# Kernel optimization log

Measured on AMD Instinct MI355X. Metric: run time of the kernel, lower is better.

The kernel has to match this reference:

```python
import jax, jax.numpy as jnp
import numpy as np

EPS = 1e-5

def _layernorm(x, g, b):
    mu = jnp.mean(x, axis=-1, keepdims=True)
    var = jnp.mean(jnp.square(x - mu), axis=-1, keepdims=True)
    return (x - mu) / jnp.sqrt(var + EPS) * g + b

def setup_inputs() -> dict:
    key = jax.random.key(0)
    ks = jax.random.split(key, 8)
    B, T, E, H, Dh, F = 4, 2048, 1024, 16, 64, 4096
    s = lambda fan: 1.0 / np.sqrt(fan)
    return {
        "x":  jax.random.normal(ks[0], (B, T, E), jnp.float32),
        "Wq": jax.random.normal(ks[1], (H, E, Dh), jnp.float32) * s(E),
        "Wk": jax.random.normal(ks[2], (H, E, Dh), jnp.float32) * s(E),
        "Wv": jax.random.normal(ks[3], (H, E, Dh), jnp.float32) * s(E),
        "Wo": jax.random.normal(ks[4], (E, E), jnp.float32) * s(E),
        "bo": jnp.zeros((E,), jnp.float32),
        "W1": jax.random.normal(ks[5], (E, F), jnp.float32) * s(E),
        "b1": jnp.zeros((F,), jnp.float32),
        "W2": jax.random.normal(ks[6], (F, E), jnp.float32) * s(F),
        "b2": jnp.zeros((E,), jnp.float32),
        "g1": jnp.ones((E,), jnp.float32),
        "bt1": jnp.zeros((E,), jnp.float32),
        "g2": jnp.ones((E,), jnp.float32),
        "bt2": jnp.zeros((E,), jnp.float32),
    }

def reference(x, Wq, Wk, Wv, Wo, bo, W1, b1, W2, b2, g1, bt1, g2, bt2):
    B, T, E = x.shape
    # --- pre-LN multi-head attention (dropout = identity in eval) ---
    h = _layernorm(x, g1, bt1)
    q = jnp.einsum('btc,hcd->bhtd', h, Wq)
    k = jnp.einsum('btc,hcd->bhtd', h, Wk)
    v = jnp.einsum('btc,hcd->bhtd', h, Wv)
    # NOTE: original scales by embed_size**-0.5 (input channel c), not head_size
    scores = jnp.einsum('bhtd,bhsd->bhts', q, k) * (E ** -0.5)
    causal = jnp.tril(jnp.ones((T, T), bool))
    scores = jnp.where(causal, scores, -jnp.inf)
    attn = jax.nn.softmax(scores, axis=-1)
    ctx = jnp.einsum('bhts,bhsd->bhtd', attn, v)
    ctx = ctx.transpose(0, 2, 1, 3).reshape(B, T, E)  # concat heads
    x = x + ctx @ Wo + bo
    # --- pre-LN feed-forward ---
    h2 = _layernorm(x, g2, bt2)
    x = x + jax.nn.relu(h2 @ W1 + b1) @ W2 + b2
    return x
```

## Files before the change

### kernel.cpp

```cpp
#include <hip/hip_runtime.h>

typedef unsigned short u16;
typedef __attribute__((ext_vector_type(8))) short bf16x8;
typedef __attribute__((ext_vector_type(4))) short bf16x4;
typedef __attribute__((ext_vector_type(4))) float f32x4;

#define LOG2E 1.4426950408889634f

__device__ __forceinline__ float b2f(u16 u) {
  union { unsigned int i; float f; } x; x.i = ((unsigned int)u) << 16; return x.f;
}
__device__ __forceinline__ u16 f2b(float f) {
  unsigned int i = __float_as_uint(f);
  unsigned int r = (i + 0x7FFFu + ((i >> 16) & 1u)) >> 16;
  return (u16)r;
}
__device__ __forceinline__ u16 f2bc(float f) {
  return (u16)((__float_as_uint(f) + 0x8000u) >> 16);
}
__device__ __forceinline__ void stc(u16* C, size_t i, float v) { C[i] = f2b(v); }
__device__ __forceinline__ void stc(float* C, size_t i, float v) { C[i] = v; }

__device__ __forceinline__ bool is_f32(const unsigned* probe) {
  return probe[0] == 0x3F800000u;
}
__device__ __forceinline__ float ldin(const void* p, size_t i, bool f32) {
  return f32 ? ((const float*)p)[i] : b2f(((const u16*)p)[i]);
}

__device__ __forceinline__ void gld_lds16(const void* g, void* l) {
  __builtin_amdgcn_global_load_lds(
      (const __attribute__((address_space(1))) unsigned int*)g,
      (__attribute__((address_space(3))) unsigned int*)l, 16, 0, 0);
}

__device__ __forceinline__ void lds_wave_fence() {
  __asm__ volatile("s_waitcnt lgkmcnt(0)" ::: "memory");
}

__device__ __forceinline__ void tr8(unsigned a[4], int lane) {
  unsigned p0, p1, p2, p3;
  p0 = __shfl_xor((int)a[0], 1, 64); p1 = __shfl_xor((int)a[1], 1, 64);
  p2 = __shfl_xor((int)a[2], 1, 64); p3 = __shfl_xor((int)a[3], 1, 64);
  unsigned sel = (lane & 1) ? 0x3276u : 0x5410u;
  a[0] = __byte_perm(a[0], p0, sel); a[1] = __byte_perm(a[1], p1, sel);
  a[2] = __byte_perm(a[2], p2, sel); a[3] = __byte_perm(a[3], p3, sel);
  p0 = __shfl_xor((int)a[0], 2, 64); p1 = __shfl_xor((int)a[1], 2, 64);
  p2 = __shfl_xor((int)a[2], 2, 64); p3 = __shfl_xor((int)a[3], 2, 64);
  if (lane & 2) { a[0] = p1; a[2] = p3; } else { a[1] = p0; a[3] = p2; }
  p0 = __shfl_xor((int)a[0], 4, 64); p1 = __shfl_xor((int)a[1], 4, 64);
  p2 = __shfl_xor((int)a[2], 4, 64); p3 = __shfl_xor((int)a[3], 4, 64);
  if (lane & 4) { a[0] = p2; a[1] = p3; } else { a[2] = p0; a[3] = p1; }
}

struct KV { bf16x8 k0, k1; unsigned va[4], vb[4]; };
__device__ __forceinline__ void load_kv(const u16* __restrict__ qkv, size_t b3072,
                                        int h, int s0, int tid, int w, int lane, KV& t) {
  t.k0 = *(const bf16x8*)(qkv + b3072 + (size_t)(s0 + (tid >> 3)) * 3072 + 1024 + h * 64 + (tid & 7) * 8);
  t.k1 = *(const bf16x8*)(qkv + b3072 + (size_t)(s0 + 32 + (tid >> 3)) * 3072 + 1024 + h * 64 + (tid & 7) * 8);
  const u16* vs = qkv + b3072 + (size_t)(s0 + lane) * 3072 + 2048 + h * 64 + w * 16;
  *(bf16x8*)t.va = *(const bf16x8*)vs;
  *(bf16x8*)t.vb = *(const bf16x8*)(vs + 8);
}

__global__ __launch_bounds__(256) void ln_kernel(
    const void* __restrict__ x, int x_raw,
    const void* __restrict__ g, const void* __restrict__ b,
    u16* __restrict__ y, const unsigned* __restrict__ probe) {
  __shared__ float red[4];
  const bool f32 = is_f32(probe);
  int row = blockIdx.x, tid = threadIdx.x;
  int w = tid >> 6;
  float f0, f1, f2, f3;
  if (x_raw && f32) {
    const float* xr = (const float*)x + (size_t)row * 1024 + tid * 4;
    float4 v = *(const float4*)xr;
    f0 = v.x; f1 = v.y; f2 = v.z; f3 = v.w;
  } else {
    const u16* xr = (const u16*)x + (size_t)row * 1024 + tid * 4;
    bf16x4 v = *(const bf16x4*)xr;
    f0 = b2f((u16)v[0]); f1 = b2f((u16)v[1]); f2 = b2f((u16)v[2]); f3 = b2f((u16)v[3]);
  }
  float s = f0 + f1 + f2 + f3;
  #pragma unroll
  for (int o = 32; o >= 1; o >>= 1) s += __shfl_xor(s, o, 64);
  if ((tid & 63) == 0) red[w] = s;
  __syncthreads();
  float mean = (red[0] + red[1] + red[2] + red[3]) * (1.0f / 1024.0f);
  __syncthreads();
  float d0 = f0 - mean, d1 = f1 - mean, d2 = f2 - mean, d3 = f3 - mean;
  float vs = d0 * d0 + d1 * d1 + d2 * d2 + d3 * d3;
  #pragma unroll
  for (int o = 32; o >= 1; o >>= 1) vs += __shfl_xor(vs, o, 64);
  if ((tid & 63) == 0) red[w] = vs;
  __syncthreads();
  float var = (red[0] + red[1] + red[2] + red[3]) * (1.0f / 1024.0f);
  float rstd = rsqrtf(var + 1e-5f);
  int c = tid * 4;
  float o0 = d0 * rstd * ldin(g, c + 0, f32) + ldin(b, c + 0, f32);
  float o1 = d1 * rstd * ldin(g, c + 1, f32) + ldin(b, c + 1, f32);
  float o2 = d2 * rstd * ldin(g, c + 2, f32) + ldin(b, c + 2, f32);
  float o3 = d3 * rstd * ldin(g, c + 3, f32) + ldin(b, c + 3, f32);
  bf16x4 ov; ov[0] = (short)f2b(o0); ov[1] = (short)f2b(o1);
  ov[2] = (short)f2b(o2); ov[3] = (short)f2b(o3);
  *(bf16x4*)(y + (size_t)row * 1024 + c) = ov;
}

__global__ __launch_bounds__(256) void repack_t(
    const void* __restrict__ src, u16* __restrict__ dst, int N, int K,
    const unsigned* __restrict__ probe) {
  const bool f32 = is_f32(probe);
  int flat = blockIdx.x * 256 + threadIdx.x;
  int n = flat % N;
  int c0 = (flat / N) * 8;
  bf16x8 t;
  #pragma unroll
  for (int j = 0; j < 8; j++) t[j] = (short)f2b(ldin(src, (size_t)(c0 + j) * N + n, f32));
  *(bf16x8*)&dst[(size_t)n * K + c0] = t;
}

__global__ __launch_bounds__(256) void repack_qkv(
    const void* __restrict__ Wq, const void* __restrict__ Wk,
    const void* __restrict__ Wv, u16* __restrict__ dst,
    const unsigned* __restrict__ probe) {
  const bool f32 = is_f32(probe);
  int flat = blockIdx.x * 256 + threadIdx.x;
  int n = flat % 3072;
  int c0 = (flat / 3072) * 8;
  const void* W = (n < 1024) ? Wq : (n < 2048) ? Wk : Wv;
  int nn = n & 1023;
  int hn = nn >> 6, d = nn & 63;
  bf16x8 t;
  #pragma unroll
  for (int j = 0; j < 8; j++)
    t[j] = (short)f2b(ldin(W, (size_t)hn * 65536 + (size_t)(c0 + j) * 64 + d, f32));
  *(bf16x8*)&dst[(size_t)n * 1024 + c0] = t;
}

template <int EPI, typename CT>
__global__ __launch_bounds__(256) void gemm_bt(
    const u16* __restrict__ A, const u16* __restrict__ Bt, CT* __restrict__ C,
    int M, int N, int K, const void* __restrict__ bias,
    const void* __restrict__ res, int res_raw,
    const unsigned* __restrict__ probe) {
  __shared__ __align__(16) u16 sA[128 * 32];
  __shared__ __align__(16) u16 sB[128 * 32];
  const bool f32 = is_f32(probe);
  int tid = threadIdx.x;
  int w = tid >> 6, lane = tid & 63;
  int l15 = lane & 15, q4 = lane >> 4;
  int bm = blockIdx.x * 128, bn = blockIdx.y * 128;
  int wm = (w & 1) * 64, wn = (w >> 1) * 64;
  f32x4 acc[4][4] = {};
  for (int k0 = 0; k0 < K; k0 += 32) {
    #pragma unroll
    for (int j = 0; j < 2; ++j) {
      int c = j * 256 + tid;
      int row = c >> 2, ck = (c & 3) * 8;
      gld_lds16(A + (size_t)(bm + row) * K + k0 + ck, &sA[c * 8]);
    }
    #pragma unroll
    for (int j = 0; j < 2; ++j) {
      int c = j * 256 + tid;
      int row = c >> 2, ck = (c & 3) * 8;
      gld_lds16(Bt + (size_t)(bn + row) * K + k0 + ck, &sB[c * 8]);
    }
    __syncthreads();
    bf16x8 af[4], bf[4];
    #pragma unroll
    for (int i = 0; i < 4; i++) af[i] = *(const bf16x8*)&sA[(wm + i * 16 + l15) * 32 + q4 * 8];
    #pragma unroll
    for (int j = 0; j < 4; j++) bf[j] = *(const bf16x8*)&sB[(wn + j * 16 + l15) * 32 + q4 * 8];
    #pragma unroll
    for (int i = 0; i < 4; i++)
      #pragma unroll
      for (int j = 0; j < 4; j++)
        acc[i][j] = __builtin_amdgcn_mfma_f32_16x16x32_bf16(af[i], bf[j], acc[i][j], 0, 0, 0);
    __syncthreads();
  }
  #pragma unroll
  for (int i = 0; i < 4; i++) {
    int rg = bm + wm + i * 16 + q4 * 4;
    #pragma unroll
    for (int j = 0; j < 4; j++) {
      int cg = bn + wn + j * 16 + l15;
      float bv = (EPI > 0) ? ldin(bias, cg, f32) : 0.0f;
      #pragma unroll
      for (int r = 0; r < 4; r++) {
        float v = acc[i][j][r];
        if (EPI == 1) v += bv + ldin(res, (size_t)(rg + r) * N + cg, res_raw && f32);
        if (EPI == 2) { v += bv; v = fmaxf(v, 0.0f); }
        stc(C, (size_t)(rg + r) * N + cg, v);
      }
    }
  }
}

__global__ __launch_bounds__(256, 4) void attn_kernel(
    const u16* __restrict__ qkv, u16* __restrict__ ctx, int T) {
  __shared__ __align__(16) u16 sK[64 * 68];
  __shared__ __align__(16) u16 sVt[80 * 68];
  __shared__ __align__(16) u16 sP[4 * 16 * 68];
  int tid = threadIdx.x;
  int w = tid >> 6, lane = tid & 63;
  int l15 = lane & 15, q4 = lane >> 4;
  int n = blockIdx.x;
  int qp = n & 15, h = (n >> 4) & 15, b = n >> 8;
  size_t b3072 = (size_t)(b * T) * 3072;
  int pbase = w * 1088;
  const float C = 0.03125f * LOG2E;

  for (int i = tid; i < 16 * 64; i += 256)
    sVt[(64 + (i >> 6)) * 68 + (i & 63)] = 0x3F80;

  KV cur, nxt;
  load_kv(qkv, b3072, h, 0, tid, w, lane, cur);

  for (int half = 0; half < 2; ++half) {
    int qt = half ? (31 - qp) : qp;
    int mb = qt * 64 + w * 16;
    bf16x8 qf0, qf1;
    {
      const u16* qr = qkv + b3072 + (size_t)(mb + l15) * 3072 + h * 64;
      qf0 = *(const bf16x8*)(qr + q4 * 8);
      qf1 = *(const bf16x8*)(qr + 32 + q4 * 8);
    }
    f32x4 o[5] = {};
    int L = qt + 1;
    for (int kt = 0; kt < L; ++kt) {
      int s0 = kt * 64;
      __syncthreads();
      *(bf16x8*)&sK[(tid >> 3) * 68 + (tid & 7) * 8] = cur.k0;
      *(bf16x8*)&sK[(32 + (tid >> 3)) * 68 + (tid & 7) * 8] = cur.k1;
      tr8(cur.va, lane); tr8(cur.vb, lane);
      {
        int dd = w * 16 + (lane & 7), t0 = (lane >> 3) * 8;
        *(bf16x8*)&sVt[dd * 68 + t0] = *(bf16x8*)cur.va;
        *(bf16x8*)&sVt[(dd + 8) * 68 + t0] = *(bf16x8*)cur.vb;
      }
      __syncthreads();
      int ns0 = (kt + 1 < L) ? s0 + 64 : 0;
      load_kv(qkv, b3072, h, ns0, tid, w, lane, nxt);

      bool diag = (kt == qt);
      #pragma unroll
      for (int j = 0; j < 4; ++j) {
        bf16x8 k0 = *(const bf16x8*)&sK[(j * 16 + l15) * 68 + q4 * 8];
        bf16x8 k1 = *(const bf16x8*)&sK[(j * 16 + l15) * 68 + 32 + q4 * 8];
        f32x4 z = {0.f, 0.f, 0.f, 0.f};
        z = __builtin_amdgcn_mfma_f32_16x16x32_bf16(qf0, k0, z, 0, 0, 0);
        z = __builtin_amdgcn_mfma_f32_16x16x32_bf16(qf1, k1, z, 0, 0, 0);
        #pragma unroll
        for (int r = 0; r < 4; ++r) {
          float p = __builtin_amdgcn_exp2f(z[r] * C);
          if (diag && (s0 + j * 16 + l15 > mb + q4 * 4 + r)) p = 0.f;
          sP[pbase + (q4 * 4 + r) * 68 + j * 16 + l15] = f2bc(p);
        }
      }
      lds_wave_fence();
      bf16x8 pf0 = *(const bf16x8*)&sP[pbase + l15 * 68 + q4 * 8];
      bf16x8 pf1 = *(const bf16x8*)&sP[pbase + l15 * 68 + 32 + q4 * 8];
      #pragma unroll
      for (int j = 0; j < 5; ++j) {
        bf16x8 vf0 = *(const bf16x8*)&sVt[(j * 16 + l15) * 68 + q4 * 8];
        bf16x8 vf1 = *(const bf16x8*)&sVt[(j * 16 + l15) * 68 + 32 + q4 * 8];
        o[j] = __builtin_amdgcn_mfma_f32_16x16x32_bf16(pf0, vf0, o[j], 0, 0, 0);
        o[j] = __builtin_amdgcn_mfma_f32_16x16x32_bf16(pf1, vf1, o[j], 0, 0, 0);
      }
      cur = nxt;
    }
    float inv[4];
    #pragma unroll
    for (int r = 0; r < 4; ++r) inv[r] = 1.0f / o[4][r];
    #pragma unroll
    for (int j = 0; j < 4; ++j)
      #pragma unroll
      for (int r = 0; r < 4; ++r) {
        size_t addr = (size_t)(b * T + mb + q4 * 4 + r) * 1024 + h * 64 + j * 16 + l15;
        ctx[addr] = f2b(o[j][r] * inv[r]);
      }
  }
}

extern "C" void kernel_launch(void* const* d_in, const int* in_sizes, int n_in,
                              void* d_out, int out_size, void* d_ws, size_t ws_size,
                              hipStream_t stream) {
  (void)in_sizes; (void)n_in; (void)out_size; (void)ws_size;
  const void* x   = d_in[0];
  const void* Wq  = d_in[1];
  const void* Wk  = d_in[2];
  const void* Wv  = d_in[3];
  const void* Wo  = d_in[4];
  const void* bo  = d_in[5];
  const void* W1  = d_in[6];
  const void* b1  = d_in[7];
  const void* W2  = d_in[8];
  const void* b2  = d_in[9];
  const void* g1  = d_in[10];
  const void* bt1 = d_in[11];
  const void* g2  = d_in[12];
  const void* bt2 = d_in[13];
  const unsigned* probe = (const unsigned*)g1;
  float* out = (float*)d_out;

  const int BT = 8192, T = 2048;
  char* ws = (char*)d_ws;
  u16* hln    = (u16*)(ws);
  u16* qkv    = (u16*)(ws + 16777216);
  u16* ctx    = (u16*)(ws + 16777216 + 50331648);
  u16* a      = (u16*)(ws + 16777216);
  u16* x1     = (u16*)(ws + 83886080);
  u16* wqkv_t = (u16*)(ws + 100663296);
  u16* wo_t   = (u16*)(ws + 106954752);
  u16* w1_t   = (u16*)(ws + 109051904);
  u16* w2_t   = (u16*)(ws + 117440512);

  repack_qkv<<<1536, 256, 0, stream>>>(Wq, Wk, Wv, wqkv_t, probe);
  repack_t<<<512, 256, 0, stream>>>(Wo, wo_t, 1024, 1024, probe);
  repack_t<<<2048, 256, 0, stream>>>(W1, w1_t, 4096, 1024, probe);
  repack_t<<<2048, 256, 0, stream>>>(W2, w2_t, 1024, 4096, probe);

  ln_kernel<<<BT, 256, 0, stream>>>(x, 1, g1, bt1, hln, probe);
  gemm_bt<0, u16><<<dim3(64, 24), 256, 0, stream>>>(hln, wqkv_t, qkv, BT, 3072, 1024,
                                                    nullptr, nullptr, 0, probe);
  attn_kernel<<<1024, 256, 0, stream>>>(qkv, ctx, T);
  gemm_bt<1, u16><<<dim3(64, 8), 256, 0, stream>>>(ctx, wo_t, x1, BT, 1024, 1024,
                                                   bo, x, 1, probe);
  ln_kernel<<<BT, 256, 0, stream>>>(x1, 0, g2, bt2, hln, probe);
  gemm_bt<2, u16><<<dim3(64, 32), 256, 0, stream>>>(hln, w1_t, a, BT, 4096, 1024,
                                                    b1, nullptr, 0, probe);
  gemm_bt<1, float><<<dim3(64, 8), 256, 0, stream>>>(a, w2_t, out, BT, 1024, 4096,
                                                     b2, x1, 0, probe);
}
```

Before: 726.2 us.

## Process two 64-row query tiles per attention block to reuse K/V tiles

```diff
diff --git a/kernel.cpp b/kernel.cpp
--- a/kernel.cpp
+++ b/kernel.cpp
@@ -196,7 +196,7 @@
   }
 }
 
-__global__ __launch_bounds__(256, 4) void attn_kernel(
+__global__ __launch_bounds__(256, 2) void attn_kernel(
     const u16* __restrict__ qkv, u16* __restrict__ ctx, int T) {
   __shared__ __align__(16) u16 sK[64 * 68];
   __shared__ __align__(16) u16 sVt[80 * 68];
@@ -205,7 +205,7 @@
   int w = tid >> 6, lane = tid & 63;
   int l15 = lane & 15, q4 = lane >> 4;
   int n = blockIdx.x;
-  int qp = n & 15, h = (n >> 4) & 15, b = n >> 8;
+  int qp = n & 7, h = (n >> 3) & 15, b = n >> 7;
   size_t b3072 = (size_t)(b * T) * 3072;
   int pbase = w * 1088;
   const float C = 0.03125f * LOG2E;
@@ -217,16 +217,20 @@
   load_kv(qkv, b3072, h, 0, tid, w, lane, cur);
 
   for (int half = 0; half < 2; ++half) {
-    int qt = half ? (31 - qp) : qp;
-    int mb = qt * 64 + w * 16;
-    bf16x8 qf0, qf1;
+    int qt = half ? (15 - qp) : qp;
+    int qt0 = qt * 128;
+    int mb0 = qt0 + w * 16, mb1 = qt0 + 64 + w * 16;
+    bf16x8 qf[2][2];
     {
-      const u16* qr = qkv + b3072 + (size_t)(mb + l15) * 3072 + h * 64;
-      qf0 = *(const bf16x8*)(qr + q4 * 8);
-      qf1 = *(const bf16x8*)(qr + 32 + q4 * 8);
-    }
-    f32x4 o[5] = {};
-    int L = qt + 1;
+      const u16* qr0 = qkv + b3072 + (size_t)(mb0 + l15) * 3072 + h * 64;
+      qf[0][0] = *(const bf16x8*)(qr0 + q4 * 8);
+      qf[0][1] = *(const bf16x8*)(qr0 + 32 + q4 * 8);
+      const u16* qr1 = qkv + b3072 + (size_t)(mb1 + l15) * 3072 + h * 64;
+      qf[1][0] = *(const bf16x8*)(qr1 + q4 * 8);
+      qf[1][1] = *(const bf16x8*)(qr1 + 32 + q4 * 8);
+    }
+    f32x4 o[2][5] = {};
+    int L = 2 * qt + 2;
     for (int kt = 0; kt < L; ++kt) {
       int s0 = kt * 64;
       __syncthreads();
@@ -242,43 +246,66 @@
       int ns0 = (kt + 1 < L) ? s0 + 64 : 0;
       load_kv(qkv, b3072, h, ns0, tid, w, lane, nxt);
 
-      bool diag = (kt == qt);
+      bool act0 = (s0 <= mb0 + 15);
+      f32x4 s[2][4];
       #pragma unroll
       for (int j = 0; j < 4; ++j) {
         bf16x8 k0 = *(const bf16x8*)&sK[(j * 16 + l15) * 68 + q4 * 8];
         bf16x8 k1 = *(const bf16x8*)&sK[(j * 16 + l15) * 68 + 32 + q4 * 8];
+        if (act0) {
+          f32x4 z = {0.f, 0.f, 0.f, 0.f};
+          z = __builtin_amdgcn_mfma_f32_16x16x32_bf16(qf[0][0], k0, z, 0, 0, 0);
+          s[0][j] = __builtin_amdgcn_mfma_f32_16x16x32_bf16(qf[0][1], k1, z, 0, 0, 0);
+        }
         f32x4 z = {0.f, 0.f, 0.f, 0.f};
-        z = __builtin_amdgcn_mfma_f32_16x16x32_bf16(qf0, k0, z, 0, 0, 0);
-        z = __builtin_amdgcn_mfma_f32_16x16x32_bf16(qf1, k1, z, 0, 0, 0);
+        z = __builtin_amdgcn_mfma_f32_16x16x32_bf16(qf[1][0], k0, z, 0, 0, 0);
+        s[1][j] = __builtin_amdgcn_mfma_f32_16x16x32_bf16(qf[1][1], k1, z, 0, 0, 0);
+      }
+      bf16x8 pf[2][2];
+      #pragma unroll
+      for (int m = 0; m < 2; ++m) {
+        if (m == 0 && !act0) continue;
+        int mbm = m ? mb1 : mb0;
+        bool dg = (s0 + 63 > mbm);
         #pragma unroll
-        for (int r = 0; r < 4; ++r) {
-          float p = __builtin_amdgcn_exp2f(z[r] * C);
-          if (diag && (s0 + j * 16 + l15 > mb + q4 * 4 + r)) p = 0.f;
-          sP[pbase + (q4 * 4 + r) * 68 + j * 16 + l15] = f2bc(p);
-        }
-      }
-      lds_wave_fence();
-      bf16x8 pf0 = *(const bf16x8*)&sP[pbase + l15 * 68 + q4 * 8];
-      bf16x8 pf1 = *(const bf16x8*)&sP[pbase + l15 * 68 + 32 + q4 * 8];
+        for (int j = 0; j < 4; ++j)
+          #pragma unroll
+          for (int r = 0; r < 4; ++r) {
+            float p = __builtin_amdgcn_exp2f(s[m][j][r] * C);
+            if (dg && (s0 + j * 16 + l15 > mbm + q4 * 4 + r)) p = 0.f;
+            sP[pbase + (q4 * 4 + r) * 68 + j * 16 + l15] = f2bc(p);
+          }
+        lds_wave_fence();
+        pf[m][0] = *(const bf16x8*)&sP[pbase + l15 * 68 + q4 * 8];
+        pf[m][1] = *(const bf16x8*)&sP[pbase + l15 * 68 + 32 + q4 * 8];
+      }
       #pragma unroll
       for (int j = 0; j < 5; ++j) {
         bf16x8 vf0 = *(const bf16x8*)&sVt[(j * 16 + l15) * 68 + q4 * 8];
         bf16x8 vf1 = *(const bf16x8*)&sVt[(j * 16 + l15) * 68 + 32 + q4 * 8];
-        o[j] = __builtin_amdgcn_mfma_f32_16x16x32_bf16(pf0, vf0, o[j], 0, 0, 0);
-        o[j] = __builtin_amdgcn_mfma_f32_16x16x32_bf16(pf1, vf1, o[j], 0, 0, 0);
+        if (act0) {
+          o[0][j] = __builtin_amdgcn_mfma_f32_16x16x32_bf16(pf[0][0], vf0, o[0][j], 0, 0, 0);
+          o[0][j] = __builtin_amdgcn_mfma_f32_16x16x32_bf16(pf[0][1], vf1, o[0][j], 0, 0, 0);
+        }
+        o[1][j] = __builtin_amdgcn_mfma_f32_16x16x32_bf16(pf[1][0], vf0, o[1][j], 0, 0, 0);
+        o[1][j] = __builtin_amdgcn_mfma_f32_16x16x32_bf16(pf[1][1], vf1, o[1][j], 0, 0, 0);
       }
       cur = nxt;
     }
-    float inv[4];
-    #pragma unroll
-    for (int r = 0; r < 4; ++r) inv[r] = 1.0f / o[4][r];
-    #pragma unroll
-    for (int j = 0; j < 4; ++j)
-      #pragma unroll
-      for (int r = 0; r < 4; ++r) {
-        size_t addr = (size_t)(b * T + mb + q4 * 4 + r) * 1024 + h * 64 + j * 16 + l15;
-        ctx[addr] = f2b(o[j][r] * inv[r]);
-      }
+    #pragma unroll
+    for (int m = 0; m < 2; ++m) {
+      int mbm = m ? mb1 : mb0;
+      float inv[4];
+      #pragma unroll
+      for (int r = 0; r < 4; ++r) inv[r] = 1.0f / o[m][4][r];
+      #pragma unroll
+      for (int j = 0; j < 4; ++j)
+        #pragma unroll
+        for (int r = 0; r < 4; ++r) {
+          size_t addr = (size_t)(b * T + mbm + q4 * 4 + r) * 1024 + h * 64 + j * 16 + l15;
+          ctx[addr] = f2b(o[m][j][r] * inv[r]);
+        }
+    }
   }
 }
 
@@ -323,7 +350,7 @@
   ln_kernel<<<BT, 256, 0, stream>>>(x, 1, g1, bt1, hln, probe);
   gemm_bt<0, u16><<<dim3(64, 24), 256, 0, stream>>>(hln, wqkv_t, qkv, BT, 3072, 1024,
                                                     nullptr, nullptr, 0, probe);
-  attn_kernel<<<1024, 256, 0, stream>>>(qkv, ctx, T);
+  attn_kernel<<<512, 256, 0, stream>>>(qkv, ctx, T);
   gemm_bt<1, u16><<<dim3(64, 8), 256, 0, stream>>>(ctx, wo_t, x1, BT, 1024, 1024,
                                                    bo, x, 1, probe);
   ln_kernel<<<BT, 256, 0, stream>>>(x1, 0, g2, bt2, hln, probe);
```

After: 673.0 us. 1.08x faster.
